# Performance work log

Measured on AMD Instinct MI355X. Metric: run time of the kernel, lower is better.

## Reference

```python
import jax, jax.numpy as jnp
import numpy as np

B, L, D, Q, H = 16, 2048, 1024, 1024, 256
NEG_NUM = -10000.0


def setup_inputs() -> dict:
    key = jax.random.key(0)
    ks = jax.random.split(key, 8)
    ctx = jax.random.normal(ks[0], (B, L, D), dtype=jnp.float32)
    query = jax.random.normal(ks[1], (B, Q), dtype=jnp.float32)
    mask = jax.random.randint(ks[2], (B, L), 0, 2, dtype=jnp.int32)
    # lin_in2proj: Linear(D+Q, H)
    lim1 = 1.0 / np.sqrt(D + Q)
    W1 = jax.random.uniform(ks[3], (H, D + Q), jnp.float32, -lim1, lim1)
    b1 = jax.random.uniform(ks[4], (H,), jnp.float32, -lim1, lim1)
    # lin_proj2score: weight_norm(Linear(H, 1)), dim=0 -> g scalar per row
    lim2 = 1.0 / np.sqrt(H)
    v = jax.random.uniform(ks[5], (1, H), jnp.float32, -lim2, lim2)
    g = jnp.linalg.norm(v).reshape(1, 1)  # weight_norm init: g = ||v||
    b2 = jax.random.uniform(ks[6], (1,), jnp.float32, -lim2, lim2)
    return {"ctx": ctx, "query": query, "mask": mask,
            "W1": W1, "b1": b1, "v": v, "g": g, "b2": b2}


def reference(ctx, query, mask, W1, b1, v, g, b2):
    d = ctx.shape[-1]
    # concat([ctx, query_expanded]) @ W1^T == ctx @ W1c^T + query @ W1q^T
    Wc, Wq = W1[:, :d], W1[:, d:]
    hid = jnp.tanh(jnp.einsum('bld,hd->blh', ctx, Wc)
                   + jnp.einsum('bq,hq->bh', query, Wq)[:, None, :]
                   + b1)                                 # (B, L, H)
    w2 = (g * v / jnp.linalg.norm(v))[0]                 # weight-normed row (H,)
    score = jnp.einsum('blh,h->bl', hid, w2) + b2[0]     # (B, L)
    score = jnp.where(mask == 1, NEG_NUM, score)
    p_ctx = jax.nn.softmax(score, axis=-1)               # (B, L)
    expected_ctx = jnp.einsum('bl,bld->bd', p_ctx, ctx)  # (B, D)
    return expected_ctx, p_ctx
```

## Files before the change

kernel.cpp:

```cpp
#include <hip/hip_runtime.h>
#include <hip/hip_bf16.h>

#define BB 16
#define LCTX 2048
#define DDIM 1024
#define QDIM 1024
#define HDIM 256
#define NEGV -10000.0f

typedef __attribute__((ext_vector_type(8))) short short8;
typedef __attribute__((ext_vector_type(4))) float f32x4;

__device__ inline unsigned short f2bf(float x) {
    unsigned int u = __float_as_uint(x);
    unsigned int r = (u + 0x7fffu + ((u >> 16) & 1u)) >> 16;
    return (unsigned short)r;
}

__global__ __launch_bounds__(256) void k_prep(const float* __restrict__ query,
                                              const float* __restrict__ W1,
                                              const float* __restrict__ b1,
                                              const float* __restrict__ v,
                                              const float* __restrict__ g,
                                              float* __restrict__ qproj,
                                              unsigned short* __restrict__ Wc_sw,
                                              float* __restrict__ w2) {
    int bid = blockIdx.x;
    if (bid < 1024) {
        int b = bid >> 6;
        int hq = bid & 63;
        int wid = threadIdx.x >> 6, lane = threadIdx.x & 63;
        int h = hq * 4 + wid;
        const float* q = query + b * QDIM;
        const float* w = W1 + (size_t)h * (DDIM + QDIM) + DDIM;
        float s = 0.f;
        #pragma unroll 4
        for (int k = lane; k < QDIM; k += 64) s += q[k] * w[k];
        #pragma unroll
        for (int o = 32; o; o >>= 1) s += __shfl_down(s, o);
        if (lane == 0) qproj[b * HDIM + h] = s + b1[h];
    } else if (bid < 1280) {
        int h = bid - 1024;
        const float* src = W1 + (size_t)h * (DDIM + QDIM);
        int hx = h & 7;
        for (int d = threadIdx.x; d < DDIM; d += 256) {
            int kt = d >> 6;
            int s  = (d >> 3) & 7;
            int dl = d & 7;
            int dp = (kt << 6) + ((s ^ hx) << 3) + dl;
            Wc_sw[h * DDIM + dp] = f2bf(src[d]);
        }
    } else {
        __shared__ float red[256];
        float vv = (threadIdx.x < HDIM) ? v[threadIdx.x] : 0.f;
        red[threadIdx.x] = vv * vv;
        __syncthreads();
        for (int o = 128; o; o >>= 1) {
            if (threadIdx.x < o) red[threadIdx.x] += red[threadIdx.x + o];
            __syncthreads();
        }
        float nrm = sqrtf(red[0]);
        if (threadIdx.x < HDIM) w2[threadIdx.x] = g[0] * vv / nrm;
    }
}

__global__ __launch_bounds__(256, 2) void k_score(const float* __restrict__ ctx,
                                                  const unsigned short* __restrict__ Wc_sw,
                                                  const float* __restrict__ qproj,
                                                  const float* __restrict__ w2,
                                                  const float* __restrict__ b2,
                                                  const int* __restrict__ mask,
                                                  float* __restrict__ e_ws,
                                                  float* __restrict__ esum_ws,
                                                  float* __restrict__ part) {
    __shared__ unsigned short Wt[2][256 * 64];
    __shared__ unsigned short At[2][64 * 64];
    int tid = threadIdx.x;
    int wid = tid >> 6, lane = tid & 63;
    int hl = lane & 15, lhi = lane >> 4;
    int bid = blockIdx.x;
    int row0 = bid * 64;
    int b = row0 >> 11;
    int wrow0 = wid * 64;

    f32x4 acc[4][4];
    #pragma unroll
    for (int mt = 0; mt < 4; mt++)
        #pragma unroll
        for (int ht = 0; ht < 4; ht++)
            acc[mt][ht] = (f32x4){0.f, 0.f, 0.f, 0.f};

    int srow = tid >> 2;
    int c0 = (tid & 3) * 2;
    int sx = srow & 7;
    const float* csrc = ctx + (size_t)(row0 + srow) * DDIM + (tid & 3) * 16;

    float4 a0, a1, a2, a3, b0, b1, b2v, b3;

#define STAGE_W(BUF, KT) do { \
    _Pragma("unroll") \
    for (int i_ = 0; i_ < 8; i_++) { \
        const unsigned short* gsrc_ = Wc_sw + (size_t)(wrow0 + i_ * 8 + (lane >> 3)) * DDIM + (KT) * 64 + (lane & 7) * 8; \
        __builtin_amdgcn_global_load_lds( \
            (const __attribute__((address_space(1))) unsigned int*)gsrc_, \
            (__attribute__((address_space(3))) unsigned int*)(&Wt[BUF][(wrow0 + i_ * 8) * 64]), \
            16, 0, 0); \
    } } while (0)

#define CTX_ISSUE(KT, R0, R1, R2, R3) do { \
    const float* cp_ = csrc + (KT) * 64; \
    R0 = *(const float4*)(cp_ + 0);  R1 = *(const float4*)(cp_ + 4); \
    R2 = *(const float4*)(cp_ + 8);  R3 = *(const float4*)(cp_ + 12); } while (0)

#define WRITE_A(BUF, U0, U1, U2, U3) do { \
    short8 p0_ = { (short)f2bf(U0.x), (short)f2bf(U0.y), (short)f2bf(U0.z), (short)f2bf(U0.w), \
                   (short)f2bf(U1.x), (short)f2bf(U1.y), (short)f2bf(U1.z), (short)f2bf(U1.w) }; \
    short8 p1_ = { (short)f2bf(U2.x), (short)f2bf(U2.y), (short)f2bf(U2.z), (short)f2bf(U2.w), \
                   (short)f2bf(U3.x), (short)f2bf(U3.y), (short)f2bf(U3.z), (short)f2bf(U3.w) }; \
    *(short8*)(&At[BUF][srow * 64 + (((c0 + 0) ^ sx) << 3)]) = p0_; \
    *(short8*)(&At[BUF][srow * 64 + (((c0 + 1) ^ sx) << 3)]) = p1_; } while (0)

#define COMPUTE(BUF) do { \
    __builtin_amdgcn_s_setprio(1); \
    _Pragma("unroll") \
    for (int ks_ = 0; ks_ < 2; ks_++) { \
        int s_ = ks_ * 4 + lhi; \
        int xc_ = (s_ ^ (hl & 7)) << 3; \
        short8 af_[4], bf_[4]; \
        _Pragma("unroll") \
        for (int mt_ = 0; mt_ < 4; mt_++) \
            af_[mt_] = *(const short8*)(&At[BUF][(mt_ * 16 + hl) * 64 + xc_]); \
        _Pragma("unroll") \
        for (int ht_ = 0; ht_ < 4; ht_++) \
            bf_[ht_] = *(const short8*)(&Wt[BUF][(wrow0 + ht_ * 16 + hl) * 64 + xc_]); \
        _Pragma("unroll") \
        for (int mt_ = 0; mt_ < 4; mt_++) \
            _Pragma("unroll") \
            for (int ht_ = 0; ht_ < 4; ht_++) \
                acc[mt_][ht_] = __builtin_amdgcn_mfma_f32_16x16x32_bf16(af_[mt_], bf_[ht_], acc[mt_][ht_], 0, 0, 0); \
    } \
    __builtin_amdgcn_s_setprio(0); } while (0)

#define BODY(T, R0, R1, R2, R3, U0, U1, U2, U3) do { \
    STAGE_W(((T) + 1) & 1, ((T) + 1) & 15); \
    __builtin_amdgcn_sched_barrier(0); \
    CTX_ISSUE(((T) + 2) & 15, R0, R1, R2, R3); \
    __builtin_amdgcn_sched_barrier(0); \
    asm volatile("s_waitcnt vmcnt(16)" ::: "memory"); \
    __builtin_amdgcn_sched_barrier(0); \
    COMPUTE((T) & 1); \
    asm volatile("s_waitcnt vmcnt(12)" ::: "memory"); \
    __builtin_amdgcn_sched_barrier(0); \
    WRITE_A(((T) + 1) & 1, U0, U1, U2, U3); \
    asm volatile("s_waitcnt lgkmcnt(0)" ::: "memory"); \
    __builtin_amdgcn_s_barrier(); \
    __builtin_amdgcn_sched_barrier(0); } while (0)

    CTX_ISSUE(0, a0, a1, a2, a3);
    __builtin_amdgcn_sched_barrier(0);
    STAGE_W(0, 0);
    __builtin_amdgcn_sched_barrier(0);
    asm volatile("s_waitcnt vmcnt(8)" ::: "memory");
    __builtin_amdgcn_sched_barrier(0);
    WRITE_A(0, a0, a1, a2, a3);
    CTX_ISSUE(1, b0, b1, b2v, b3);
    asm volatile("s_waitcnt lgkmcnt(0)" ::: "memory");
    __builtin_amdgcn_s_barrier();
    __builtin_amdgcn_sched_barrier(0);

    BODY(0,  a0, a1, a2, a3,  b0, b1, b2v, b3);
    BODY(1,  b0, b1, b2v, b3, a0, a1, a2, a3);
    BODY(2,  a0, a1, a2, a3,  b0, b1, b2v, b3);
    BODY(3,  b0, b1, b2v, b3, a0, a1, a2, a3);
    BODY(4,  a0, a1, a2, a3,  b0, b1, b2v, b3);
    BODY(5,  b0, b1, b2v, b3, a0, a1, a2, a3);
    BODY(6,  a0, a1, a2, a3,  b0, b1, b2v, b3);
    BODY(7,  b0, b1, b2v, b3, a0, a1, a2, a3);
    BODY(8,  a0, a1, a2, a3,  b0, b1, b2v, b3);
    BODY(9,  b0, b1, b2v, b3, a0, a1, a2, a3);
    BODY(10, a0, a1, a2, a3,  b0, b1, b2v, b3);
    BODY(11, b0, b1, b2v, b3, a0, a1, a2, a3);
    BODY(12, a0, a1, a2, a3,  b0, b1, b2v, b3);
    BODY(13, b0, b1, b2v, b3, a0, a1, a2, a3);
    BODY(14, a0, a1, a2, a3,  b0, b1, b2v, b3);
    BODY(15, b0, b1, b2v, b3, a0, a1, a2, a3);

    float qp[4], wv[4];
    #pragma unroll
    for (int ht = 0; ht < 4; ht++) {
        int h = wrow0 + ht * 16 + hl;
        qp[ht] = qproj[b * HDIM + h];
        wv[ht] = w2[h];
    }
    float* sb  = (float*)At;
    float* sbe = sb + 256;
    #pragma unroll
    for (int mt = 0; mt < 4; mt++) {
        #pragma unroll
        for (int r = 0; r < 4; r++) {
            float partial = 0.f;
            #pragma unroll
            for (int ht = 0; ht < 4; ht++) {
                float x = acc[mt][ht][r] + qp[ht];
                x = fminf(fmaxf(x, -15.f), 15.f);
                float e = __expf(2.f * x);
                partial += (e - 1.f) / (e + 1.f) * wv[ht];
            }
            #pragma unroll
            for (int o = 1; o < 16; o <<= 1) partial += __shfl_xor(partial, o);
            if (hl == 0) sb[wid * 64 + mt * 16 + lhi * 4 + r] = partial;
        }
    }
    __syncthreads();

    if (tid < 64) {
        float s = sb[tid] + sb[64 + tid] + sb[128 + tid] + sb[192 + tid] + b2[0];
        int grow = row0 + tid;
        int bb = grow >> 11, ll = grow & 2047;
        float e = (mask[bb * 2048 + ll] == 1) ? 0.f : __expf(s);
        e_ws[grow] = e;
        sbe[tid] = e;
        float tot = e;
        #pragma unroll
        for (int o = 32; o; o >>= 1) tot += __shfl_down(tot, o);
        if (tid == 0) esum_ws[bid] = tot;
    }
    __syncthreads();

    {
        int d0 = tid * 4;
        const float* cb = ctx + (size_t)row0 * DDIM + d0;
        float4 a = {0.f, 0.f, 0.f, 0.f};
        #pragma unroll 8
        for (int l = 0; l < 64; l++) {
            float el = sbe[l];
            float4 cc = *(const float4*)(cb + (size_t)l * DDIM);
            a.x += el * cc.x; a.y += el * cc.y; a.z += el * cc.z; a.w += el * cc.w;
        }
        *(float4*)(part + (size_t)bid * DDIM + d0) = a;
    }
}

__global__ __launch_bounds__(256) void k_norm(const float* __restrict__ e_ws,
                                              const float* __restrict__ esum_ws,
                                              const float* __restrict__ part,
                                              float* __restrict__ out_exp,
                                              float* __restrict__ out_p) {
    int b = blockIdx.x, dc = blockIdx.y;
    int tid = threadIdx.x;
    float se = 0.f;
    #pragma unroll
    for (int j = 0; j < 32; j++) se += esum_ws[b * 32 + j];
    float inv = 1.f / se;
    if (tid < 128) {
        int d = dc * 128 + tid;
        float s = 0.f;
        #pragma unroll
        for (int j = 0; j < 32; j++) s += part[(size_t)(b * 32 + j) * DDIM + d];
        out_exp[b * DDIM + d] = s * inv;
    }
    int l = dc * 256 + tid;
    out_p[b * LCTX + l] = e_ws[b * LCTX + l] * inv;
}

extern "C" void kernel_launch(void* const* d_in, const int* in_sizes, int n_in,
                              void* d_out, int out_size, void* d_ws, size_t ws_size,
                              hipStream_t stream) {
    const float* ctx   = (const float*)d_in[0];
    const float* query = (const float*)d_in[1];
    const int*   mask  = (const int*)d_in[2];
    const float* W1    = (const float*)d_in[3];
    const float* b1    = (const float*)d_in[4];
    const float* v     = (const float*)d_in[5];
    const float* g     = (const float*)d_in[6];
    const float* b2    = (const float*)d_in[7];
    float* out_exp = (float*)d_out;
    float* out_p   = (float*)d_out + 16384;

    char* ws = (char*)d_ws;
    unsigned short* Wc_sw = (unsigned short*)ws;
    float* qproj = (float*)(ws + 524288);
    float* w2    = (float*)(ws + 540672);
    float* e_ws  = (float*)(ws + 541696);
    float* esum  = (float*)(ws + 672768);
    float* part  = (float*)(ws + 674816);

    k_prep <<<dim3(1281),   256, 0, stream>>>(query, W1, b1, v, g, qproj, Wc_sw, w2);
    k_score<<<dim3(512),    256, 0, stream>>>(ctx, Wc_sw, qproj, w2, b2, mask, e_ws, esum, part);
    k_norm <<<dim3(16, 8),  256, 0, stream>>>(e_ws, esum, part, out_exp, out_p);
}
```

Baseline: 59.87 us.

## Split score GEMM by rows per wave with ctx fragments loaded straight to registers

The score kernel's wave decomposition changes. Each wave used to own 64 H columns for all 64 rows, reading A tiles from LDS. Now each wave owns 16 rows across all 256 H columns, and loads its ctx A fragment directly from global into registers, converting to bf16 there, so the A staging through LDS and its LDS writes disappear. The per-row score reduction across waves is also removed, which drops one block barrier and the shared reduction buffer. In exchange, each wave reads the full W tile from LDS, so LDS read traffic per MFMA rises. The accumulator count and the per-lane qproj and w2 registers also grow, which may raise register pressure and affect occupancy at two blocks per CU.

After: 60.65 us. Within noise of the previous version (+1.3%).

```diff
diff --git a/kernel.cpp b/kernel.cpp
--- a/kernel.cpp
+++ b/kernel.cpp
@@ -68,164 +68,125 @@
                                                   const unsigned short* __restrict__ Wc_sw,
                                                   const float* __restrict__ qproj,
                                                   const float* __restrict__ w2,
-                                                  const float* __restrict__ b2,
+                                                  const float* __restrict__ b2p,
                                                   const int* __restrict__ mask,
                                                   float* __restrict__ e_ws,
                                                   float* __restrict__ esum_ws,
                                                   float* __restrict__ part) {
     __shared__ unsigned short Wt[2][256 * 64];
-    __shared__ unsigned short At[2][64 * 64];
+    __shared__ float sbe[64];
     int tid = threadIdx.x;
     int wid = tid >> 6, lane = tid & 63;
     int hl = lane & 15, lhi = lane >> 4;
-    int bid = blockIdx.x;
-    int row0 = bid * 64;
+    int row0 = blockIdx.x * 64;
     int b = row0 >> 11;
-    int wrow0 = wid * 64;
-
-    f32x4 acc[4][4];
-    #pragma unroll
-    for (int mt = 0; mt < 4; mt++)
-        #pragma unroll
-        for (int ht = 0; ht < 4; ht++)
-            acc[mt][ht] = (f32x4){0.f, 0.f, 0.f, 0.f};
-
-    int srow = tid >> 2;
-    int c0 = (tid & 3) * 2;
-    int sx = srow & 7;
-    const float* csrc = ctx + (size_t)(row0 + srow) * DDIM + (tid & 3) * 16;
-
-    float4 a0, a1, a2, a3, b0, b1, b2v, b3;
+
+    f32x4 acc[16];
+    #pragma unroll
+    for (int ht = 0; ht < 16; ht++) acc[ht] = (f32x4){0.f, 0.f, 0.f, 0.f};
+
+    const float* abase = ctx + (size_t)(row0 + wid * 16 + hl) * DDIM + lhi * 8;
+
+    float4 r0, r1, r2, r3, s0, s1, s2, s3;
 
 #define STAGE_W(BUF, KT) do { \
     _Pragma("unroll") \
     for (int i_ = 0; i_ < 8; i_++) { \
-        const unsigned short* gsrc_ = Wc_sw + (size_t)(wrow0 + i_ * 8 + (lane >> 3)) * DDIM + (KT) * 64 + (lane & 7) * 8; \
+        const unsigned short* gsrc_ = Wc_sw + (size_t)(wid * 64 + i_ * 8 + (lane >> 3)) * DDIM + (KT) * 64 + (lane & 7) * 8; \
         __builtin_amdgcn_global_load_lds( \
             (const __attribute__((address_space(1))) unsigned int*)gsrc_, \
-            (__attribute__((address_space(3))) unsigned int*)(&Wt[BUF][(wrow0 + i_ * 8) * 64]), \
+            (__attribute__((address_space(3))) unsigned int*)(&Wt[BUF][(wid * 64 + i_ * 8) * 64]), \
             16, 0, 0); \
     } } while (0)
 
-#define CTX_ISSUE(KT, R0, R1, R2, R3) do { \
-    const float* cp_ = csrc + (KT) * 64; \
-    R0 = *(const float4*)(cp_ + 0);  R1 = *(const float4*)(cp_ + 4); \
-    R2 = *(const float4*)(cp_ + 8);  R3 = *(const float4*)(cp_ + 12); } while (0)
-
-#define WRITE_A(BUF, U0, U1, U2, U3) do { \
-    short8 p0_ = { (short)f2bf(U0.x), (short)f2bf(U0.y), (short)f2bf(U0.z), (short)f2bf(U0.w), \
-                   (short)f2bf(U1.x), (short)f2bf(U1.y), (short)f2bf(U1.z), (short)f2bf(U1.w) }; \
-    short8 p1_ = { (short)f2bf(U2.x), (short)f2bf(U2.y), (short)f2bf(U2.z), (short)f2bf(U2.w), \
-                   (short)f2bf(U3.x), (short)f2bf(U3.y), (short)f2bf(U3.z), (short)f2bf(U3.w) }; \
-    *(short8*)(&At[BUF][srow * 64 + (((c0 + 0) ^ sx) << 3)]) = p0_; \
-    *(short8*)(&At[BUF][srow * 64 + (((c0 + 1) ^ sx) << 3)]) = p1_; } while (0)
-
-#define COMPUTE(BUF) do { \
+#define ISSUE_A(KT, R0, R1, R2, R3) do { \
+    const float* p_ = abase + (KT) * 64; \
+    R0 = *(const float4*)(p_ + 0);  R1 = *(const float4*)(p_ + 4); \
+    R2 = *(const float4*)(p_ + 32); R3 = *(const float4*)(p_ + 36); } while (0)
+
+#define BODY(KT, R0, R1, R2, R3, S0, S1, S2, S3) do { \
+    asm volatile("s_waitcnt vmcnt(4)" ::: "memory"); \
+    __builtin_amdgcn_s_barrier(); \
+    __builtin_amdgcn_sched_barrier(0); \
+    if ((KT) < 15) { \
+        STAGE_W(((KT) + 1) & 1, (KT) + 1); \
+        ISSUE_A((KT) + 1, S0, S1, S2, S3); \
+        __builtin_amdgcn_sched_barrier(0); \
+    } \
+    short8 af0_ = { (short)f2bf(R0.x), (short)f2bf(R0.y), (short)f2bf(R0.z), (short)f2bf(R0.w), \
+                    (short)f2bf(R1.x), (short)f2bf(R1.y), (short)f2bf(R1.z), (short)f2bf(R1.w) }; \
+    short8 af1_ = { (short)f2bf(R2.x), (short)f2bf(R2.y), (short)f2bf(R2.z), (short)f2bf(R2.w), \
+                    (short)f2bf(R3.x), (short)f2bf(R3.y), (short)f2bf(R3.z), (short)f2bf(R3.w) }; \
     __builtin_amdgcn_s_setprio(1); \
     _Pragma("unroll") \
-    for (int ks_ = 0; ks_ < 2; ks_++) { \
-        int s_ = ks_ * 4 + lhi; \
-        int xc_ = (s_ ^ (hl & 7)) << 3; \
-        short8 af_[4], bf_[4]; \
-        _Pragma("unroll") \
-        for (int mt_ = 0; mt_ < 4; mt_++) \
-            af_[mt_] = *(const short8*)(&At[BUF][(mt_ * 16 + hl) * 64 + xc_]); \
-        _Pragma("unroll") \
-        for (int ht_ = 0; ht_ < 4; ht_++) \
-            bf_[ht_] = *(const short8*)(&Wt[BUF][(wrow0 + ht_ * 16 + hl) * 64 + xc_]); \
-        _Pragma("unroll") \
-        for (int mt_ = 0; mt_ < 4; mt_++) \
-            _Pragma("unroll") \
-            for (int ht_ = 0; ht_ < 4; ht_++) \
-                acc[mt_][ht_] = __builtin_amdgcn_mfma_f32_16x16x32_bf16(af_[mt_], bf_[ht_], acc[mt_][ht_], 0, 0, 0); \
+    for (int ht_ = 0; ht_ < 16; ht_++) { \
+        short8 bf0_ = *(const short8*)(&Wt[(KT) & 1][(ht_ * 16 + hl) * 64 + ((lhi ^ (hl & 7)) << 3)]); \
+        acc[ht_] = __builtin_amdgcn_mfma_f32_16x16x32_bf16(af0_, bf0_, acc[ht_], 0, 0, 0); \
+    } \
+    _Pragma("unroll") \
+    for (int ht_ = 0; ht_ < 16; ht_++) { \
+        short8 bf1_ = *(const short8*)(&Wt[(KT) & 1][(ht_ * 16 + hl) * 64 + (((4 + lhi) ^ (hl & 7)) << 3)]); \
+        acc[ht_] = __builtin_amdgcn_mfma_f32_16x16x32_bf16(af1_, bf1_, acc[ht_], 0, 0, 0); \
     } \
     __builtin_amdgcn_s_setprio(0); } while (0)
 
-#define BODY(T, R0, R1, R2, R3, U0, U1, U2, U3) do { \
-    STAGE_W(((T) + 1) & 1, ((T) + 1) & 15); \
-    __builtin_amdgcn_sched_barrier(0); \
-    CTX_ISSUE(((T) + 2) & 15, R0, R1, R2, R3); \
-    __builtin_amdgcn_sched_barrier(0); \
-    asm volatile("s_waitcnt vmcnt(16)" ::: "memory"); \
-    __builtin_amdgcn_sched_barrier(0); \
-    COMPUTE((T) & 1); \
-    asm volatile("s_waitcnt vmcnt(12)" ::: "memory"); \
-    __builtin_amdgcn_sched_barrier(0); \
-    WRITE_A(((T) + 1) & 1, U0, U1, U2, U3); \
-    asm volatile("s_waitcnt lgkmcnt(0)" ::: "memory"); \
-    __builtin_amdgcn_s_barrier(); \
-    __builtin_amdgcn_sched_barrier(0); } while (0)
-
-    CTX_ISSUE(0, a0, a1, a2, a3);
+    STAGE_W(0, 0);
+    ISSUE_A(0, r0, r1, r2, r3);
     __builtin_amdgcn_sched_barrier(0);
-    STAGE_W(0, 0);
-    __builtin_amdgcn_sched_barrier(0);
-    asm volatile("s_waitcnt vmcnt(8)" ::: "memory");
-    __builtin_amdgcn_sched_barrier(0);
-    WRITE_A(0, a0, a1, a2, a3);
-    CTX_ISSUE(1, b0, b1, b2v, b3);
-    asm volatile("s_waitcnt lgkmcnt(0)" ::: "memory");
-    __builtin_amdgcn_s_barrier();
-    __builtin_amdgcn_sched_barrier(0);
-
-    BODY(0,  a0, a1, a2, a3,  b0, b1, b2v, b3);
-    BODY(1,  b0, b1, b2v, b3, a0, a1, a2, a3);
-    BODY(2,  a0, a1, a2, a3,  b0, b1, b2v, b3);
-    BODY(3,  b0, b1, b2v, b3, a0, a1, a2, a3);
-    BODY(4,  a0, a1, a2, a3,  b0, b1, b2v, b3);
-    BODY(5,  b0, b1, b2v, b3, a0, a1, a2, a3);
-    BODY(6,  a0, a1, a2, a3,  b0, b1, b2v, b3);
-    BODY(7,  b0, b1, b2v, b3, a0, a1, a2, a3);
-    BODY(8,  a0, a1, a2, a3,  b0, b1, b2v, b3);
-    BODY(9,  b0, b1, b2v, b3, a0, a1, a2, a3);
-    BODY(10, a0, a1, a2, a3,  b0, b1, b2v, b3);
-    BODY(11, b0, b1, b2v, b3, a0, a1, a2, a3);
-    BODY(12, a0, a1, a2, a3,  b0, b1, b2v, b3);
-    BODY(13, b0, b1, b2v, b3, a0, a1, a2, a3);
-    BODY(14, a0, a1, a2, a3,  b0, b1, b2v, b3);
-    BODY(15, b0, b1, b2v, b3, a0, a1, a2, a3);
-
-    float qp[4], wv[4];
-    #pragma unroll
-    for (int ht = 0; ht < 4; ht++) {
-        int h = wrow0 + ht * 16 + hl;
-        qp[ht] = qproj[b * HDIM + h];
-        wv[ht] = w2[h];
-    }
-    float* sb  = (float*)At;
-    float* sbe = sb + 256;
-    #pragma unroll
-    for (int mt = 0; mt < 4; mt++) {
-        #pragma unroll
-        for (int r = 0; r < 4; r++) {
-            float partial = 0.f;
-            #pragma unroll
-            for (int ht = 0; ht < 4; ht++) {
-                float x = acc[mt][ht][r] + qp[ht];
-                x = fminf(fmaxf(x, -15.f), 15.f);
-                float e = __expf(2.f * x);
-                partial += (e - 1.f) / (e + 1.f) * wv[ht];
-            }
-            #pragma unroll
-            for (int o = 1; o < 16; o <<= 1) partial += __shfl_xor(partial, o);
-            if (hl == 0) sb[wid * 64 + mt * 16 + lhi * 4 + r] = partial;
+
+    BODY(0,  r0, r1, r2, r3, s0, s1, s2, s3);
+    BODY(1,  s0, s1, s2, s3, r0, r1, r2, r3);
+    BODY(2,  r0, r1, r2, r3, s0, s1, s2, s3);
+    BODY(3,  s0, s1, s2, s3, r0, r1, r2, r3);
+    BODY(4,  r0, r1, r2, r3, s0, s1, s2, s3);
+    BODY(5,  s0, s1, s2, s3, r0, r1, r2, r3);
+    BODY(6,  r0, r1, r2, r3, s0, s1, s2, s3);
+    BODY(7,  s0, s1, s2, s3, r0, r1, r2, r3);
+    BODY(8,  r0, r1, r2, r3, s0, s1, s2, s3);
+    BODY(9,  s0, s1, s2, s3, r0, r1, r2, r3);
+    BODY(10, r0, r1, r2, r3, s0, s1, s2, s3);
+    BODY(11, s0, s1, s2, s3, r0, r1, r2, r3);
+    BODY(12, r0, r1, r2, r3, s0, s1, s2, s3);
+    BODY(13, s0, s1, s2, s3, r0, r1, r2, r3);
+    BODY(14, r0, r1, r2, r3, s0, s1, s2, s3);
+    BODY(15, s0, s1, s2, s3, r0, r1, r2, r3);
+
+    float qp[16], wv[16];
+    #pragma unroll
+    for (int ht = 0; ht < 16; ht++) {
+        qp[ht] = qproj[b * HDIM + ht * 16 + hl];
+        wv[ht] = w2[ht * 16 + hl];
+    }
+    float bias2 = b2p[0];
+    #pragma unroll
+    for (int r = 0; r < 4; r++) {
+        float partial = 0.f;
+        #pragma unroll
+        for (int ht = 0; ht < 16; ht++) {
+            float x = acc[ht][r] + qp[ht];
+            x = fminf(fmaxf(x, -15.f), 15.f);
+            float e2 = __expf(2.f * x);
+            partial += (e2 - 1.f) / (e2 + 1.f) * wv[ht];
+        }
+        #pragma unroll
+        for (int o = 1; o < 16; o <<= 1) partial += __shfl_xor(partial, o);
+        if (hl == 0) {
+            int lrow = wid * 16 + lhi * 4 + r;
+            int grow = row0 + lrow;
+            float s = partial + bias2;
+            float e = (mask[b * 2048 + (grow & 2047)] == 1) ? 0.f : __expf(s);
+            e_ws[grow] = e;
+            sbe[lrow] = e;
         }
     }
     __syncthreads();
 
     if (tid < 64) {
-        float s = sb[tid] + sb[64 + tid] + sb[128 + tid] + sb[192 + tid] + b2[0];
-        int grow = row0 + tid;
-        int bb = grow >> 11, ll = grow & 2047;
-        float e = (mask[bb * 2048 + ll] == 1) ? 0.f : __expf(s);
-        e_ws[grow] = e;
-        sbe[tid] = e;
-        float tot = e;
+        float tot = sbe[tid];
         #pragma unroll
         for (int o = 32; o; o >>= 1) tot += __shfl_down(tot, o);
-        if (tid == 0) esum_ws[bid] = tot;
-    }
-    __syncthreads();
+        if (tid == 0) esum_ws[blockIdx.x] = tot;
+    }
 
     {
         int d0 = tid * 4;
@@ -237,7 +198,7 @@
             float4 cc = *(const float4*)(cb + (size_t)l * DDIM);
             a.x += el * cc.x; a.y += el * cc.y; a.z += el * cc.z; a.w += el * cc.w;
         }
-        *(float4*)(part + (size_t)bid * DDIM + d0) = a;
+        *(float4*)(part + (size_t)blockIdx.x * DDIM + d0) = a;
     }
 }
 
```
